# Optimization experiments

Hardware: AMD Instinct MI355X
Metric: run time of the kernel (lower is better)

## Reference

```python
import jax, jax.numpy as jnp
import numpy as np


def setup_inputs() -> dict:
    key = jax.random.key(0)
    k1, k2 = jax.random.split(key)
    pred_corners = jax.random.normal(k1, (2048, 8, 3), dtype=jnp.float32)
    gt_corners = jax.random.normal(k2, (2048, 8, 3), dtype=jnp.float32)
    return {"pred_corners": pred_corners, "gt_corners": gt_corners}


def _chamfer(pred_corners, gt_corners):
    # flatten boxes -> point clouds: [Np*8, 3], [Ng*8, 3]
    x = pred_corners.reshape(-1, 3)
    y = gt_corners.reshape(-1, 3)
    x2 = jnp.sum(x * x, axis=-1)  # [N]
    y2 = jnp.sum(y * y, axis=-1)  # [M]
    d2 = x2[:, None] + y2[None, :] - 2.0 * jnp.einsum("nd,md->nm", x, y)
    dist = jnp.sqrt(jnp.maximum(d2, 0.0))  # [N, M]
    # bidirectional min, averaged per box (8 corners) then over boxes
    min_p2g = jnp.min(dist, axis=1).reshape(-1, 8).mean(axis=1)
    min_g2p = jnp.min(dist, axis=0).reshape(-1, 8).mean(axis=1)
    return min_p2g.mean() + min_g2p.mean()


def reference(pred_corners, gt_corners):
    return _chamfer(pred_corners, gt_corners)
```

## Files before the change

kernel.cpp:

```cpp
#include <hip/hip_runtime.h>


#define NPTS   16384
#define RPT    8
#define BLOCK  256
#define XPB    (RPT * BLOCK)
#define NXB    (NPTS / XPB)
#define NSEG   64
#define YSEG   (NPTS / NSEG)
#define NPART  (2 * NSEG * NPTS)
#define K2B    128
#define WS_NEED ((NPART + K2B) * 4)


__global__ __launch_bounds__(BLOCK, 4) void chamfer_partial(
        const float* __restrict__ pred, const float* __restrict__ gt,
        float* __restrict__ part) {
    const int xb  = blockIdx.x;
    const int ys  = blockIdx.y;
    const int dir = blockIdx.z;
    const float* __restrict__ X = dir ? gt : pred;
    const float* __restrict__ Y = dir ? pred : gt;
    const int tid = threadIdx.x;

    __shared__ float4 sh[YSEG];
    {
        int yi = ys * YSEG + tid;
        float a = Y[3 * yi + 0], b = Y[3 * yi + 1], c = Y[3 * yi + 2];
        sh[tid] = make_float4(a, b, c, -0.5f * (a * a + b * b + c * c));
    }

    float xx[RPT], xy[RPT], xz[RPT], x2[RPT], mx[RPT];
    const int xbase = xb * XPB;
#pragma unroll
    for (int r = 0; r < RPT; ++r) {
        int xi = xbase + r * BLOCK + tid;
        xx[r] = X[3 * xi + 0];
        xy[r] = X[3 * xi + 1];
        xz[r] = X[3 * xi + 2];
        x2[r] = xx[r] * xx[r] + xy[r] * xy[r] + xz[r] * xz[r];
        mx[r] = -3.0e38f;
    }

    __syncthreads();

#pragma unroll 2
    for (int j = 0; j < YSEG; j += 2) {
        float4 y0 = sh[j];
        float4 y1 = sh[j + 1];
#pragma unroll
        for (int r = 0; r < RPT; ++r) {
            float t0 = fmaf(xz[r], y0.z, y0.w);
            t0 = fmaf(xy[r], y0.y, t0);
            t0 = fmaf(xx[r], y0.x, t0);
            float t1 = fmaf(xz[r], y1.z, y1.w);
            t1 = fmaf(xy[r], y1.y, t1);
            t1 = fmaf(xx[r], y1.x, t1);
            mx[r] = fmaxf(mx[r], fmaxf(t0, t1));
        }
    }

    float* __restrict__ dst = part + (dir * NSEG + ys) * NPTS;
#pragma unroll
    for (int r = 0; r < RPT; ++r) {
        int xi = xbase + r * BLOCK + tid;
        dst[xi] = fmaf(-2.0f, mx[r], x2[r]);
    }
}

__global__ __launch_bounds__(256) void chamfer_combine(
        const float* __restrict__ part, float* __restrict__ sums) {
    const int gid = blockIdx.x * 256 + threadIdx.x;
    const int dir = gid >> 14;
    const int x   = gid & (NPTS - 1);
    float m = 3.0e38f;
#pragma unroll 8
    for (int s = 0; s < NSEG; ++s)
        m = fminf(m, part[(dir * NSEG + s) * NPTS + x]);
    float v = sqrtf(fmaxf(m, 0.0f));

#pragma unroll
    for (int off = 32; off > 0; off >>= 1)
        v += __shfl_down(v, off, 64);

    __shared__ float lsum[4];
    if ((threadIdx.x & 63) == 0) lsum[threadIdx.x >> 6] = v;
    __syncthreads();
    if (threadIdx.x == 0)
        sums[blockIdx.x] = lsum[0] + lsum[1] + lsum[2] + lsum[3];
}

__global__ __launch_bounds__(128) void chamfer_final(
        const float* __restrict__ sums, float* __restrict__ out) {
    float v = sums[threadIdx.x];
#pragma unroll
    for (int off = 32; off > 0; off >>= 1)
        v += __shfl_down(v, off, 64);
    __shared__ float w[2];
    if ((threadIdx.x & 63) == 0) w[threadIdx.x >> 6] = v;
    __syncthreads();
    if (threadIdx.x == 0) out[0] = (w[0] + w[1]) * (1.0f / (float)NPTS);
}


__global__ __launch_bounds__(256) void init_mins(unsigned int* mins, float* out) {
    int i = blockIdx.x * blockDim.x + threadIdx.x;
    if (i < 2 * NPTS) mins[i] = 0x7F800000u;
    if (i == 0) out[0] = 0.0f;
}

__global__ __launch_bounds__(BLOCK, 4) void chamfer_min_atomic(
        const float* __restrict__ pred, const float* __restrict__ gt,
        unsigned int* __restrict__ mins) {
    const int xb  = blockIdx.x;
    const int ys  = blockIdx.y;
    const int dir = blockIdx.z;
    const float* __restrict__ X = dir ? gt : pred;
    const float* __restrict__ Y = dir ? pred : gt;
    unsigned int* __restrict__ outm = mins + dir * NPTS;
    const int tid = threadIdx.x;

    __shared__ float4 sh[YSEG];
    {
        int yi = ys * YSEG + tid;
        float a = Y[3 * yi + 0], b = Y[3 * yi + 1], c = Y[3 * yi + 2];
        sh[tid] = make_float4(a, b, c, -0.5f * (a * a + b * b + c * c));
    }
    float xx[RPT], xy[RPT], xz[RPT], x2[RPT], mx[RPT];
    const int xbase = xb * XPB;
#pragma unroll
    for (int r = 0; r < RPT; ++r) {
        int xi = xbase + r * BLOCK + tid;
        xx[r] = X[3 * xi + 0];
        xy[r] = X[3 * xi + 1];
        xz[r] = X[3 * xi + 2];
        x2[r] = xx[r] * xx[r] + xy[r] * xy[r] + xz[r] * xz[r];
        mx[r] = -3.0e38f;
    }
    __syncthreads();
#pragma unroll 2
    for (int j = 0; j < YSEG; j += 2) {
        float4 y0 = sh[j], y1 = sh[j + 1];
#pragma unroll
        for (int r = 0; r < RPT; ++r) {
            float t0 = fmaf(xz[r], y0.z, y0.w);
            t0 = fmaf(xy[r], y0.y, t0);
            t0 = fmaf(xx[r], y0.x, t0);
            float t1 = fmaf(xz[r], y1.z, y1.w);
            t1 = fmaf(xy[r], y1.y, t1);
            t1 = fmaf(xx[r], y1.x, t1);
            mx[r] = fmaxf(mx[r], fmaxf(t0, t1));
        }
    }
#pragma unroll
    for (int r = 0; r < RPT; ++r) {
        int xi = xbase + r * BLOCK + tid;
        float d2 = fmaxf(fmaf(-2.0f, mx[r], x2[r]), 0.0f);
        atomicMin(&outm[xi], __float_as_uint(d2));
    }
}

__global__ __launch_bounds__(256) void chamfer_reduce_atomic(
        const unsigned int* __restrict__ mins, float* __restrict__ out) {
    const int gid = blockIdx.x * 256 + threadIdx.x;
    float s = 0.0f;
#pragma unroll
    for (int i = 0; i < 2; ++i)
        s += sqrtf(__uint_as_float(mins[gid + i * 64 * 256]));
#pragma unroll
    for (int off = 32; off > 0; off >>= 1)
        s += __shfl_down(s, off, 64);
    if ((threadIdx.x & 63) == 0)
        atomicAdd(out, s * (1.0f / (float)NPTS));
}

extern "C" void kernel_launch(void* const* d_in, const int* in_sizes, int n_in,
                              void* d_out, int out_size, void* d_ws, size_t ws_size,
                              hipStream_t stream) {
    const float* pred = (const float*)d_in[0];
    const float* gt   = (const float*)d_in[1];
    float* out        = (float*)d_out;

    if (ws_size >= (size_t)WS_NEED) {
        float* part = (float*)d_ws;
        float* sums = part + NPART;
        hipLaunchKernelGGL(chamfer_partial, dim3(NXB, NSEG, 2), dim3(BLOCK), 0,
                           stream, pred, gt, part);
        hipLaunchKernelGGL(chamfer_combine, dim3(K2B), dim3(256), 0, stream,
                           part, sums);
        hipLaunchKernelGGL(chamfer_final, dim3(1), dim3(128), 0, stream,
                           sums, out);
    } else {
        unsigned int* mins = (unsigned int*)d_ws;
        hipLaunchKernelGGL(init_mins, dim3((2 * NPTS + 255) / 256), dim3(256), 0,
                           stream, mins, out);
        hipLaunchKernelGGL(chamfer_min_atomic, dim3(NXB, NSEG, 2), dim3(BLOCK), 0,
                           stream, pred, gt, mins);
        hipLaunchKernelGGL(chamfer_reduce_atomic, dim3(64), dim3(256), 0, stream,
                           mins, out);
    }
}
```

Baseline: 110.0 us.

## Fuse chamfer partial/combine/final into single atomic-min kernel with last-block reduction

Replaces the three-kernel pipeline, which wrote a large per-segment partial buffer and then reduced it, with one kernel. It folds per-segment minima into a small buffer through unsigned atomicMin, and a ticket counter lets the last block to finish compute the sqrt sum. The workspace is initialized by a memset (0xFF bytes, with the ticket wrapping from 0xFFFFFFFF). The kernel also doubles rows per thread and segments, which raises register pressure and lowers LDS use. The aim is to remove heavy partial-buffer traffic and extra launches, at the cost of atomic contention and a serialized final reduction in one block.

```diff
diff --git a/kernel.cpp b/kernel.cpp
--- a/kernel.cpp
+++ b/kernel.cpp
@@ -2,32 +2,33 @@
 
 
 #define NPTS   16384
-#define RPT    8
+#define RPT    16
 #define BLOCK  256
 #define XPB    (RPT * BLOCK)
 #define NXB    (NPTS / XPB)
-#define NSEG   64
+#define NSEG   128
 #define YSEG   (NPTS / NSEG)
-#define NPART  (2 * NSEG * NPTS)
-#define K2B    128
-#define WS_NEED ((NPART + K2B) * 4)
+#define GRID   (2 * NXB * NSEG)
+#define WS_NEED (2 * NPTS * 4 + 4)
 
-
-__global__ __launch_bounds__(BLOCK, 4) void chamfer_partial(
+__global__ __launch_bounds__(BLOCK, 4) void chamfer_fused(
         const float* __restrict__ pred, const float* __restrict__ gt,
-        float* __restrict__ part) {
-    const int xb  = blockIdx.x;
-    const int ys  = blockIdx.y;
-    const int dir = blockIdx.z;
+        unsigned int* __restrict__ mins, unsigned int* __restrict__ ticket,
+        float* __restrict__ out) {
+    const int b   = blockIdx.x;
+    const int dir = b >> 9;
+    const int xb  = (b >> 7) & (NXB - 1);
+    const int ys  = b & (NSEG - 1);
     const float* __restrict__ X = dir ? gt : pred;
     const float* __restrict__ Y = dir ? pred : gt;
+    unsigned int* __restrict__ outm = mins + dir * NPTS;
     const int tid = threadIdx.x;
 
     __shared__ float4 sh[YSEG];
-    {
+    if (tid < YSEG) {
         int yi = ys * YSEG + tid;
-        float a = Y[3 * yi + 0], b = Y[3 * yi + 1], c = Y[3 * yi + 2];
-        sh[tid] = make_float4(a, b, c, -0.5f * (a * a + b * b + c * c));
+        float a = Y[3 * yi + 0], bb = Y[3 * yi + 1], c = Y[3 * yi + 2];
+        sh[tid] = make_float4(a, bb, c, -0.5f * (a * a + bb * bb + c * c));
     }
 
     float xx[RPT], xy[RPT], xz[RPT], x2[RPT], mx[RPT];
@@ -44,7 +45,6 @@
 
     __syncthreads();
 
-#pragma unroll 2
     for (int j = 0; j < YSEG; j += 2) {
         float4 y0 = sh[j];
         float4 y1 = sh[j + 1];
@@ -60,46 +60,39 @@
         }
     }
 
-    float* __restrict__ dst = part + (dir * NSEG + ys) * NPTS;
 #pragma unroll
     for (int r = 0; r < RPT; ++r) {
         int xi = xbase + r * BLOCK + tid;
-        dst[xi] = fmaf(-2.0f, mx[r], x2[r]);
+        float d2 = fmaxf(fmaf(-2.0f, mx[r], x2[r]), 0.0f);
+        atomicMin(&outm[xi], __float_as_uint(d2));
     }
-}
 
-__global__ __launch_bounds__(256) void chamfer_combine(
-        const float* __restrict__ part, float* __restrict__ sums) {
-    const int gid = blockIdx.x * 256 + threadIdx.x;
-    const int dir = gid >> 14;
-    const int x   = gid & (NPTS - 1);
-    float m = 3.0e38f;
-#pragma unroll 8
-    for (int s = 0; s < NSEG; ++s)
-        m = fminf(m, part[(dir * NSEG + s) * NPTS + x]);
-    float v = sqrtf(fmaxf(m, 0.0f));
+    __shared__ bool is_last;
+    __threadfence();
+    if (tid == 0) {
+        unsigned int old = atomicAdd(ticket, 1u);
+        is_last = (old == (unsigned int)(GRID - 2));
+    }
+    __syncthreads();
 
+    if (is_last) {
+        __threadfence();
+        float s = 0.0f;
+        for (int i = tid; i < 2 * NPTS; i += BLOCK) {
+            unsigned int u = __hip_atomic_load(&mins[i], __ATOMIC_RELAXED,
+                                               __HIP_MEMORY_SCOPE_AGENT);
+            s += sqrtf(__uint_as_float(u));
+        }
 #pragma unroll
-    for (int off = 32; off > 0; off >>= 1)
-        v += __shfl_down(v, off, 64);
-
-    __shared__ float lsum[4];
-    if ((threadIdx.x & 63) == 0) lsum[threadIdx.x >> 6] = v;
-    __syncthreads();
-    if (threadIdx.x == 0)
-        sums[blockIdx.x] = lsum[0] + lsum[1] + lsum[2] + lsum[3];
-}
-
-__global__ __launch_bounds__(128) void chamfer_final(
-        const float* __restrict__ sums, float* __restrict__ out) {
-    float v = sums[threadIdx.x];
-#pragma unroll
-    for (int off = 32; off > 0; off >>= 1)
-        v += __shfl_down(v, off, 64);
-    __shared__ float w[2];
-    if ((threadIdx.x & 63) == 0) w[threadIdx.x >> 6] = v;
-    __syncthreads();
-    if (threadIdx.x == 0) out[0] = (w[0] + w[1]) * (1.0f / (float)NPTS);
+        for (int off = 32; off > 0; off >>= 1)
+            s += __shfl_down(s, off, 64);
+        __shared__ float lsum[4];
+        if ((tid & 63) == 0) lsum[tid >> 6] = s;
+        __syncthreads();
+        if (tid == 0)
+            out[0] = (lsum[0] + lsum[1] + lsum[2] + lsum[3]) *
+                     (1.0f / (float)NPTS);
+    }
 }
 
 
@@ -121,7 +114,7 @@
     const int tid = threadIdx.x;
 
     __shared__ float4 sh[YSEG];
-    {
+    if (tid < YSEG) {
         int yi = ys * YSEG + tid;
         float a = Y[3 * yi + 0], b = Y[3 * yi + 1], c = Y[3 * yi + 2];
         sh[tid] = make_float4(a, b, c, -0.5f * (a * a + b * b + c * c));
@@ -138,7 +131,6 @@
         mx[r] = -3.0e38f;
     }
     __syncthreads();
-#pragma unroll 2
     for (int j = 0; j < YSEG; j += 2) {
         float4 y0 = sh[j], y1 = sh[j + 1];
 #pragma unroll
@@ -180,18 +172,14 @@
     const float* pred = (const float*)d_in[0];
     const float* gt   = (const float*)d_in[1];
     float* out        = (float*)d_out;
+    unsigned int* mins   = (unsigned int*)d_ws;
+    unsigned int* ticket = mins + 2 * NPTS;
 
     if (ws_size >= (size_t)WS_NEED) {
-        float* part = (float*)d_ws;
-        float* sums = part + NPART;
-        hipLaunchKernelGGL(chamfer_partial, dim3(NXB, NSEG, 2), dim3(BLOCK), 0,
-                           stream, pred, gt, part);
-        hipLaunchKernelGGL(chamfer_combine, dim3(K2B), dim3(256), 0, stream,
-                           part, sums);
-        hipLaunchKernelGGL(chamfer_final, dim3(1), dim3(128), 0, stream,
-                           sums, out);
+        hipMemsetAsync(d_ws, 0xFF, (size_t)WS_NEED, stream);
+        hipLaunchKernelGGL(chamfer_fused, dim3(GRID), dim3(BLOCK), 0, stream,
+                           pred, gt, mins, ticket, out);
     } else {
-        unsigned int* mins = (unsigned int*)d_ws;
         hipLaunchKernelGGL(init_mins, dim3((2 * NPTS + 255) / 256), dim3(256), 0,
                            stream, mins, out);
         hipLaunchKernelGGL(chamfer_min_atomic, dim3(NXB, NSEG, 2), dim3(BLOCK), 0,
```

After: 173.5 us. +57.7%, slower.
